# Optimization experiments

Measured on AMD Instinct MI355X. Metric: run time of the kernel, lower is better.

The kernel has to match this reference:

```python
import jax, jax.numpy as jnp
import numpy as np

N = 20000      # nodes
E = 320000     # edges (avg degree 16)
DIN, H1, H2, DOUT = 256, 256, 128, 64


def _lin_params(key, din, dout):
    kw, kb = jax.random.split(key)
    s = 1.0 / np.sqrt(din)
    W = jax.random.uniform(kw, (din, dout), jnp.float32, -s, s)
    b = jax.random.uniform(kb, (dout,), jnp.float32, -s, s)
    return W, b


def setup_inputs() -> dict:
    key = jax.random.key(0)
    keys = jax.random.split(key, 20)
    inp = {
        'x': jax.random.normal(keys[0], (N, DIN), jnp.float32),
        'edge_index': jax.random.randint(keys[1], (2, E), 0, N, jnp.int64),
    }
    dims = [(DIN, H1), (DIN, H1), (DIN, H1),   # layer1 key/query/value
            (H1, H2), (H1, H2), (H1, H2),      # layer2
            (H2, DOUT), (H2, DOUT), (H2, DOUT)]  # layer3
    names = ['k1', 'q1', 'v1', 'k2', 'q2', 'v2', 'k3', 'q3', 'v3']
    for i, (nm, (di, do)) in enumerate(zip(names, dims)):
        W, b = _lin_params(keys[2 + i], di, do)
        inp[nm + '_w'] = W
        inp[nm + '_b'] = b
    # skip (root) weights, no bias per PyG, plus per-conv output bias
    for j, (di, do) in enumerate([(DIN, H1), (H1, H2), (H2, DOUT)], start=1):
        s = 1.0 / np.sqrt(di)
        inp[f's{j}_w'] = jax.random.uniform(keys[11 + 2 * j], (di, do), jnp.float32, -s, s)
        inp[f'bias{j}'] = jnp.zeros((do,), jnp.float32)
    return inp


def _res_gated_conv(x, src, dst, kw, kb, qw, qb, vw, vb, sw, bias):
    # PyG ResGatedGraphConv (flow source_to_target, aggr='add', act=Sigmoid):
    # out_i = lin_skip(x_i) + sum_{j->i} sigmoid(lin_key(x_i) + lin_query(x_j)) * lin_value(x_j) + bias
    k = x @ kw + kb            # [N, D]
    q = x @ qw + qb
    v = x @ vw + vb
    eta = jax.nn.sigmoid(k[dst] + q[src])   # [E, D] edge gate
    msg = eta * v[src]                      # [E, D]
    agg = jax.ops.segment_sum(msg, dst, num_segments=N)  # scatter-add to targets
    return x @ sw + agg + bias


def reference(x, edge_index,
              k1_w, k1_b, q1_w, q1_b, v1_w, v1_b,
              k2_w, k2_b, q2_w, q2_b, v2_w, v2_b,
              k3_w, k3_b, q3_w, q3_b, v3_w, v3_b,
              s1_w, bias1, s2_w, bias2, s3_w, bias3):
    src, dst = edge_index[0], edge_index[1]
    h = _res_gated_conv(x, src, dst, k1_w, k1_b, q1_w, q1_b, v1_w, v1_b, s1_w, bias1)
    # dropout (eval mode -> identity)
    h = _res_gated_conv(h, src, dst, k2_w, k2_b, q2_w, q2_b, v2_w, v2_b, s2_w, bias2)
    h = _res_gated_conv(h, src, dst, k3_w, k3_b, q3_w, q3_b, v3_w, v3_b, s3_w, bias3)
    return jax.nn.softmax(h, axis=1)
```

## Files before the change

### kernel.cpp

```cpp
#include <hip/hip_runtime.h>
#include <hip/hip_bf16.h>
#include <type_traits>


#define NN 20000
#define EE 320000
#define ELLW 64

typedef _Float16 half8 __attribute__((ext_vector_type(8)));
typedef _Float16 half4 __attribute__((ext_vector_type(4)));
typedef _Float16 half2v __attribute__((ext_vector_type(2)));
typedef float f32x4 __attribute__((ext_vector_type(4)));

__device__ __forceinline__ _Float16 f2h(float f) { return (_Float16)f; }
__device__ __forceinline__ float fsigmoid_mul(float v, float x) {
    return v * __builtin_amdgcn_rcpf(1.f + __expf(-x));
}

struct PrepArgs {
    const float* w[3][4];
    const float* b[3][4];
    _Float16* wt[3];
    float* cb[3];
};

__global__ __launch_bounds__(256) void setup_all_kernel(
    const int* __restrict__ ei, int* __restrict__ deg, int* __restrict__ flag,
    const float* __restrict__ x, _Float16* __restrict__ Xh, PrepArgs a) {
    const int b = blockIdx.x;
    const int tid = threadIdx.x;
    if (b < 79) {
        const int i = b * 256 + tid;
        if (i < NN) deg[i] = 0;
    } else if (b == 79) {
        __shared__ int nz;
        if (tid == 0) nz = 0;
        __syncthreads();
        int c = 0;
        for (int t = tid; t < 1024; t += 256)
            if (ei[2 * t + 1] != 0) c = 1;
        if (c) atomicAdd(&nz, 1);
        __syncthreads();
        if (tid == 0) *flag = (nz == 0) ? 1 : 0;
    } else if (b < 1744) {
        const int idx = (b - 80) * 256 + tid;
        int layer, li, K, D, s;
        if (idx < 262144) {
            layer = 0; li = idx; K = 256; D = 256; s = 2;
        } else if (idx < 393216) {
            layer = 1; li = idx - 262144; K = 256; D = 128; s = 1;
        } else {
            layer = 2; li = idx - 393216; K = 128; D = 64; s = 0;
        }
        const int p = li / K;
        const int k = li - p * K;
        const int DV = D >> 6;
        int grp, c;
        if (p < D) {
            grp = 0; c = p;
        } else if (p < 3 * D) {
            const int t = p - D;
            const int g = t >> (s + 1);
            const int r = t & (2 * DV - 1);
            if (r < DV) { grp = 1; c = g * DV + r; }
            else        { grp = 2; c = g * DV + r - DV; }
        } else {
            grp = 3; c = p - 3 * D;
        }
        a.wt[layer][(size_t)p * K + k] =
            f2h(a.w[layer][grp][(size_t)k * D + c]);
        if (k == 0) a.cb[layer][p] = a.b[layer][grp][c];
    } else {
        const int i = ((b - 1744) * 256 + tid) * 8;
        if (i < NN * 256) {
            const float4 f0 = *(const float4*)(x + i);
            const float4 f1 = *(const float4*)(x + i + 4);
            half8 h;
            h[0] = f2h(f0.x); h[1] = f2h(f0.y); h[2] = f2h(f0.z); h[3] = f2h(f0.w);
            h[4] = f2h(f1.x); h[5] = f2h(f1.y); h[6] = f2h(f1.z); h[7] = f2h(f1.w);
            *(half8*)(Xh + i) = h;
        }
    }
}

__device__ __forceinline__ void gemm_tile(
    int bm, int bn, const _Float16* __restrict__ A,
    const _Float16* __restrict__ Bt, const float* __restrict__ catbias,
    _Float16* __restrict__ O, int M, int K, int N) {
    __shared__ _Float16 As[2][4096];
    __shared__ _Float16 Bs[2][4096];

    const int tid = threadIdx.x;
    const int wid = tid >> 6;
    const int lane = tid & 63;
    const int tile_m = bm * 128;
    const int tile_n = bn * 128;
    const int wm = (wid & 1) * 64;
    const int wn = (wid >> 1) * 64;

    const int st_row = (wid << 4) + (lane >> 2);
    const int st_kc = (lane & 3) << 3;

    auto stage = [&](int buf, int kt) {
#pragma unroll
        for (int j = 0; j < 2; ++j) {
            int ar = tile_m + j * 64 + st_row;
            ar = ar < M ? ar : M - 1;
            const _Float16* ag = A + (size_t)ar * K + kt + st_kc;
            __builtin_amdgcn_global_load_lds(
                (const __attribute__((address_space(1))) unsigned int*)ag,
                (__attribute__((address_space(3))) unsigned int*)
                    &As[buf][j * 2048 + (wid << 9)],
                16, 0, 0);
            const int br = tile_n + j * 64 + st_row;
            const _Float16* bg = Bt + (size_t)br * K + kt + st_kc;
            __builtin_amdgcn_global_load_lds(
                (const __attribute__((address_space(1))) unsigned int*)bg,
                (__attribute__((address_space(3))) unsigned int*)
                    &Bs[buf][j * 2048 + (wid << 9)],
                16, 0, 0);
        }
    };

    stage(0, 0);

    f32x4 acc[4][4] = {};
    const int fr = lane & 15;
    const int fk = (lane >> 4) << 3;
    const int niter = K >> 5;

    for (int it = 0; it < niter; ++it) {
        __syncthreads();
        if (it + 1 < niter) stage((it + 1) & 1, (it + 1) << 5);
        const _Float16* as = As[it & 1];
        const _Float16* bs = Bs[it & 1];
        half8 af[4], bf[4];
#pragma unroll
        for (int mi = 0; mi < 4; ++mi)
            af[mi] = *(const half8*)&as[(wm + mi * 16 + fr) * 32 + fk];
#pragma unroll
        for (int ni = 0; ni < 4; ++ni)
            bf[ni] = *(const half8*)&bs[(wn + ni * 16 + fr) * 32 + fk];
#pragma unroll
        for (int mi = 0; mi < 4; ++mi)
#pragma unroll
            for (int ni = 0; ni < 4; ++ni)
                acc[mi][ni] = __builtin_amdgcn_mfma_f32_16x16x32_f16(
                    af[mi], bf[ni], acc[mi][ni], 0, 0, 0);
    }
    __syncthreads();

    _Float16* zone = &As[0][0] + wid * 2048;
    const int cl = lane & 15;
    const int rq = (lane >> 4) << 2;
    const int col0 = tile_n + wn;
    const int r0 = tile_m + wm;
#pragma unroll
    for (int mi = 0; mi < 4; ++mi) {
#pragma unroll
        for (int ni = 0; ni < 4; ++ni) {
            const float cb = catbias[col0 + ni * 16 + cl];
#pragma unroll
            for (int r = 0; r < 4; ++r)
                zone[(rq + r) * 72 + ni * 16 + cl] = f2h(acc[mi][ni][r] + cb);
        }
#pragma unroll
        for (int j = 0; j < 2; ++j) {
            const int rr = j * 8 + (lane >> 3);
            const int row = r0 + mi * 16 + rr;
            const half8 v = *(const half8*)&zone[rr * 72 + (lane & 7) * 8];
            if (row < M)
                *(half8*)&O[(size_t)row * N + col0 + (lane & 7) * 8] = v;
        }
    }
}

__global__ __launch_bounds__(256) void gemm_kernel(
    const _Float16* __restrict__ A, const _Float16* __restrict__ Bt,
    const float* __restrict__ catbias, _Float16* __restrict__ O, int M, int K,
    int N, int mblocks) {
    gemm_tile(blockIdx.x % mblocks, blockIdx.x / mblocks, A, Bt, catbias, O, M,
              K, N);
}

__global__ __launch_bounds__(256) void gemm1_fill_kernel(
    const _Float16* __restrict__ A, const _Float16* __restrict__ Bt,
    const float* __restrict__ catbias, _Float16* __restrict__ O,
    const int* __restrict__ ei, const int* __restrict__ i64flag,
    int* __restrict__ deg, int* __restrict__ col) {
    if (blockIdx.x < 1256) {
        gemm_tile(blockIdx.x % 157, blockIdx.x / 157, A, Bt, catbias, O, NN,
                  256, 1024);
        return;
    }
    const int e = (blockIdx.x - 1256) * 256 + threadIdx.x;
    if (e >= EE) return;
    int src, dst;
    if (*i64flag) {
        const long long* p = (const long long*)ei;
        src = (int)p[e];
        dst = (int)p[EE + e];
    } else {
        src = ei[e];
        dst = ei[EE + e];
    }
    const int pos = atomicAdd(&deg[dst], 1);
    if (pos < ELLW) col[dst * ELLW + pos] = src;
}

template <int D, int MODE>
__global__ __launch_bounds__(256) void edge_gather_kernel(
    const int* __restrict__ deg, const int* __restrict__ col,
    const _Float16* __restrict__ KQVS, _Float16* __restrict__ Hh,
    float* __restrict__ out, int n) {
    constexpr int DV = D / 64;
    constexpr int D4 = 4 * D;
    using qv_t = typename std::conditional<
        DV == 4, half8,
        typename std::conditional<DV == 2, half4, half2v>::type>::type;

    const int node = blockIdx.x * 4 + (threadIdx.x >> 6);
    if (node >= n) return;
    const int lane = threadIdx.x & 63;
    const int ld = lane * DV;

    int dg = deg[node];
    dg = dg < ELLW ? dg : ELLW;
    int idx = col[node * ELLW + lane];
    if (lane >= dg) idx = node;

    float k[DV], acc[DV];
    {
        const _Float16* kp = KQVS + (size_t)node * D4 + ld;
        if constexpr (DV == 4) {
            const half4 u = *(const half4*)kp;
#pragma unroll
            for (int j = 0; j < 4; ++j) k[j] = (float)u[j];
        } else if constexpr (DV == 2) {
            const half2v u = *(const half2v*)kp;
            k[0] = (float)u[0]; k[1] = (float)u[1];
        } else {
            k[0] = (float)*kp;
        }
    }
#pragma unroll
    for (int j = 0; j < DV; ++j) acc[j] = 0.f;

    const _Float16* qvbase = KQVS + D + 2 * ld;
    auto qvacc = [&](qv_t u) {
#pragma unroll
        for (int j = 0; j < DV; ++j)
            acc[j] += fsigmoid_mul((float)u[DV + j], k[j] + (float)u[j]);
    };

    for (int e = 0; e < dg; e += 8) {
        qv_t u[8];
#pragma unroll
        for (int j = 0; j < 8; ++j) {
            const int s = __shfl(idx, e + j, 64);
            u[j] = *(const qv_t*)(qvbase + (size_t)s * D4);
        }
        const int nb = dg - e;
#pragma unroll
        for (int j = 0; j < 8; ++j)
            if (j < nb) qvacc(u[j]);
    }

    float h[DV];
    {
        const _Float16* sp = KQVS + (size_t)node * D4 + 3 * D + ld;
        if constexpr (DV == 4) {
            const half4 u = *(const half4*)sp;
#pragma unroll
            for (int j = 0; j < 4; ++j) h[j] = (float)u[j] + acc[j];
        } else if constexpr (DV == 2) {
            const half2v u = *(const half2v*)sp;
            h[0] = (float)u[0] + acc[0];
            h[1] = (float)u[1] + acc[1];
        } else {
            h[0] = (float)*sp + acc[0];
        }
    }

    if constexpr (MODE == 0) {
        _Float16* op = Hh + (size_t)node * D + ld;
        if constexpr (DV == 4) {
            half4 o;
#pragma unroll
            for (int j = 0; j < 4; ++j) o[j] = f2h(h[j]);
            *(half4*)op = o;
        } else if constexpr (DV == 2) {
            half2v o;
            o[0] = f2h(h[0]); o[1] = f2h(h[1]);
            *(half2v*)op = o;
        } else {
            op[0] = f2h(h[0]);
        }
    } else {
        static_assert(MODE == 0 || DV == 1, "softmax fusion needs D==64");
        float m = h[0];
#pragma unroll
        for (int off = 32; off > 0; off >>= 1)
            m = fmaxf(m, __shfl_xor(m, off, 64));
        const float ex = __expf(h[0] - m);
        float sm = ex;
#pragma unroll
        for (int off = 32; off > 0; off >>= 1) sm += __shfl_xor(sm, off, 64);
        out[(size_t)node * 64 + lane] = ex * __builtin_amdgcn_rcpf(sm);
    }
}

extern "C" void kernel_launch(void* const* d_in, const int* in_sizes, int n_in,
                              void* d_out, int out_size, void* d_ws,
                              size_t ws_size, hipStream_t stream) {
    const float* x = (const float*)d_in[0];
    const int* ei = (const int*)d_in[1];

    char* w = (char*)d_ws;
    _Float16* Xh = (_Float16*)w;     w += (size_t)NN * 256 * 2;
    _Float16* KQVS = (_Float16*)w;   w += (size_t)NN * 1024 * 2;
    _Float16* H1h = (_Float16*)w;    w += (size_t)NN * 256 * 2;
    _Float16* H2h = (_Float16*)w;    w += (size_t)NN * 128 * 2;
    _Float16* Wt1 = (_Float16*)w;    w += (size_t)1024 * 256 * 2;
    _Float16* Wt2 = (_Float16*)w;    w += (size_t)512 * 256 * 2;
    _Float16* Wt3 = (_Float16*)w;    w += (size_t)256 * 128 * 2;
    float* cb1 = (float*)w;          w += 1024 * 4;
    float* cb2 = (float*)w;          w += 512 * 4;
    float* cb3 = (float*)w;          w += 256 * 4;
    int* i64flag = (int*)w;          w += 16;
    int* deg = (int*)w;              w += (size_t)NN * 4;
    int* ell = (int*)w;              w += (size_t)NN * ELLW * 4;

    const dim3 blk(256);
    const int gblocks = (NN + 3) / 4;

    PrepArgs pa;
    pa.w[0][0] = (const float*)d_in[2];  pa.b[0][0] = (const float*)d_in[3];
    pa.w[0][1] = (const float*)d_in[4];  pa.b[0][1] = (const float*)d_in[5];
    pa.w[0][2] = (const float*)d_in[6];  pa.b[0][2] = (const float*)d_in[7];
    pa.w[1][0] = (const float*)d_in[8];  pa.b[1][0] = (const float*)d_in[9];
    pa.w[1][1] = (const float*)d_in[10]; pa.b[1][1] = (const float*)d_in[11];
    pa.w[1][2] = (const float*)d_in[12]; pa.b[1][2] = (const float*)d_in[13];
    pa.w[2][0] = (const float*)d_in[14]; pa.b[2][0] = (const float*)d_in[15];
    pa.w[2][1] = (const float*)d_in[16]; pa.b[2][1] = (const float*)d_in[17];
    pa.w[2][2] = (const float*)d_in[18]; pa.b[2][2] = (const float*)d_in[19];
    pa.w[0][3] = (const float*)d_in[20]; pa.b[0][3] = (const float*)d_in[21];
    pa.w[1][3] = (const float*)d_in[22]; pa.b[1][3] = (const float*)d_in[23];
    pa.w[2][3] = (const float*)d_in[24]; pa.b[2][3] = (const float*)d_in[25];
    pa.wt[0] = Wt1; pa.wt[1] = Wt2; pa.wt[2] = Wt3;
    pa.cb[0] = cb1; pa.cb[1] = cb2; pa.cb[2] = cb3;

    setup_all_kernel<<<4244, blk, 0, stream>>>(ei, deg, i64flag, x, Xh, pa);

    gemm1_fill_kernel<<<2506, blk, 0, stream>>>(Xh, Wt1, cb1, KQVS, ei,
                                                i64flag, deg, ell);
    edge_gather_kernel<256, 0><<<gblocks, blk, 0, stream>>>(
        deg, ell, KQVS, H1h, nullptr, NN);

    gemm_kernel<<<157 * 4, blk, 0, stream>>>(H1h, Wt2, cb2, KQVS, NN, 256, 512,
                                             157);
    edge_gather_kernel<128, 0><<<gblocks, blk, 0, stream>>>(
        deg, ell, KQVS, H2h, nullptr, NN);

    gemm_kernel<<<157 * 2, blk, 0, stream>>>(H2h, Wt3, cb3, KQVS, NN, 128, 256,
                                             157);
    edge_gather_kernel<64, 1><<<gblocks, blk, 0, stream>>>(
        deg, ell, KQVS, nullptr, (float*)d_out, NN);
}
```

Measured before the change: 262.3 us.

## Chunk KQVS into per-32-dim column slabs and gather per chunk with 16-bit indices

The weight prep is reordered so the fused K/Q/V/S GEMM output for layers 1 and 2 lands in 128-column chunks, each stored as a contiguous [N,128] slab holding 32 dims of k, interleaved q/v and skip. New gather kernels handle one chunk per block, with 8 lanes per edge and 8 edges in flight, so each slab's random-access working set is smaller and more cache-friendly. ELL neighbour indices become unsigned short to halve index traffic. This relies on NN fitting in 16 bits and adds more blocks plus cross-lane reductions.

```diff
diff --git a/kernel.cpp b/kernel.cpp
--- a/kernel.cpp
+++ b/kernel.cpp
@@ -44,32 +44,44 @@
         if (tid == 0) *flag = (nz == 0) ? 1 : 0;
     } else if (b < 1744) {
         const int idx = (b - 80) * 256 + tid;
-        int layer, li, K, D, s;
+        int layer, li, K, D;
         if (idx < 262144) {
-            layer = 0; li = idx; K = 256; D = 256; s = 2;
+            layer = 0; li = idx; K = 256; D = 256;
         } else if (idx < 393216) {
-            layer = 1; li = idx - 262144; K = 256; D = 128; s = 1;
+            layer = 1; li = idx - 262144; K = 256; D = 128;
         } else {
-            layer = 2; li = idx - 393216; K = 128; D = 64; s = 0;
+            layer = 2; li = idx - 393216; K = 128; D = 64;
         }
         const int p = li / K;
         const int k = li - p * K;
-        const int DV = D >> 6;
-        int grp, c;
-        if (p < D) {
-            grp = 0; c = p;
-        } else if (p < 3 * D) {
-            const int t = p - D;
-            const int g = t >> (s + 1);
-            const int r = t & (2 * DV - 1);
-            if (r < DV) { grp = 1; c = g * DV + r; }
-            else        { grp = 2; c = g * DV + r - DV; }
+        int grp, dim;
+        if (layer < 2) {
+            const int c = p >> 7;
+            const int local = p & 127;
+            if (local < 32) {
+                grp = 0; dim = c * 32 + local;
+            } else if (local < 96) {
+                const int t = local - 32;
+                const int g8 = t >> 3, r = t & 7;
+                grp = (r < 4) ? 1 : 2;
+                dim = c * 32 + g8 * 4 + (r & 3);
+            } else {
+                grp = 3; dim = c * 32 + local - 96;
+            }
         } else {
-            grp = 3; c = p - 3 * D;
+            if (p < 64) {
+                grp = 0; dim = p;
+            } else if (p < 192) {
+                const int t = p - 64;
+                grp = (t & 1) ? 2 : 1;
+                dim = t >> 1;
+            } else {
+                grp = 3; dim = p - 192;
+            }
         }
         a.wt[layer][(size_t)p * K + k] =
-            f2h(a.w[layer][grp][(size_t)k * D + c]);
-        if (k == 0) a.cb[layer][p] = a.b[layer][grp][c];
+            f2h(a.w[layer][grp][(size_t)k * D + dim]);
+        if (k == 0) a.cb[layer][p] = a.b[layer][grp][dim];
     } else {
         const int i = ((b - 1744) * 256 + tid) * 8;
         if (i < NN * 256) {
@@ -83,6 +95,7 @@
     }
 }
 
+template <bool CHUNKED>
 __device__ __forceinline__ void gemm_tile(
     int bm, int bn, const _Float16* __restrict__ A,
     const _Float16* __restrict__ Bt, const float* __restrict__ catbias,
@@ -155,6 +168,16 @@
     const int rq = (lane >> 4) << 2;
     const int col0 = tile_n + wn;
     const int r0 = tile_m + wm;
+
+    _Float16* obase;
+    int ostride;
+    if constexpr (CHUNKED) {
+        obase = O + (size_t)(col0 >> 7) * NN * 128 + (col0 & 127);
+        ostride = 128;
+    } else {
+        obase = O + col0;
+        ostride = N;
+    }
 #pragma unroll
     for (int mi = 0; mi < 4; ++mi) {
 #pragma unroll
@@ -170,27 +193,28 @@
             const int row = r0 + mi * 16 + rr;
             const half8 v = *(const half8*)&zone[rr * 72 + (lane & 7) * 8];
             if (row < M)
-                *(half8*)&O[(size_t)row * N + col0 + (lane & 7) * 8] = v;
-        }
-    }
-}
-
+                *(half8*)&obase[(size_t)row * ostride + (lane & 7) * 8] = v;
+        }
+    }
+}
+
+template <bool CHUNKED>
 __global__ __launch_bounds__(256) void gemm_kernel(
     const _Float16* __restrict__ A, const _Float16* __restrict__ Bt,
     const float* __restrict__ catbias, _Float16* __restrict__ O, int M, int K,
     int N, int mblocks) {
-    gemm_tile(blockIdx.x % mblocks, blockIdx.x / mblocks, A, Bt, catbias, O, M,
-              K, N);
+    gemm_tile<CHUNKED>(blockIdx.x % mblocks, blockIdx.x / mblocks, A, Bt,
+                       catbias, O, M, K, N);
 }
 
 __global__ __launch_bounds__(256) void gemm1_fill_kernel(
     const _Float16* __restrict__ A, const _Float16* __restrict__ Bt,
     const float* __restrict__ catbias, _Float16* __restrict__ O,
     const int* __restrict__ ei, const int* __restrict__ i64flag,
-    int* __restrict__ deg, int* __restrict__ col) {
+    int* __restrict__ deg, unsigned short* __restrict__ col) {
     if (blockIdx.x < 1256) {
-        gemm_tile(blockIdx.x % 157, blockIdx.x / 157, A, Bt, catbias, O, NN,
-                  256, 1024);
+        gemm_tile<true>(blockIdx.x % 157, blockIdx.x / 157, A, Bt, catbias, O,
+                        NN, 256, 1024);
         return;
     }
     const int e = (blockIdx.x - 1256) * 256 + threadIdx.x;
@@ -205,109 +229,123 @@
         dst = ei[EE + e];
     }
     const int pos = atomicAdd(&deg[dst], 1);
-    if (pos < ELLW) col[dst * ELLW + pos] = src;
-}
-
-template <int D, int MODE>
-__global__ __launch_bounds__(256) void edge_gather_kernel(
-    const int* __restrict__ deg, const int* __restrict__ col,
-    const _Float16* __restrict__ KQVS, _Float16* __restrict__ Hh,
-    float* __restrict__ out, int n) {
-    constexpr int DV = D / 64;
-    constexpr int D4 = 4 * D;
-    using qv_t = typename std::conditional<
-        DV == 4, half8,
-        typename std::conditional<DV == 2, half4, half2v>::type>::type;
-
+    if (pos < ELLW) col[dst * ELLW + pos] = (unsigned short)src;
+}
+
+template <int NCH>
+__global__ __launch_bounds__(256) void gather_chunked_kernel(
+    const int* __restrict__ deg, const unsigned short* __restrict__ col,
+    const _Float16* __restrict__ KQVS, _Float16* __restrict__ Hh, int n) {
+    const int b = blockIdx.x;
+    int chunk, group;
+    if constexpr (NCH == 8) {
+        chunk = b & 7;
+        group = b >> 3;
+    } else {
+        const int slot = b & 7;
+        chunk = slot & 3;
+        group = ((b >> 3) << 1) | (slot >> 2);
+    }
+    const int wid = threadIdx.x >> 6;
+    const int node = group * 4 + wid;
+    if (node >= n) return;
+    const int lane = threadIdx.x & 63;
+    const int j = lane & 7;
+    const int g = lane >> 3;
+
+    const _Float16* cbase = KQVS + (size_t)chunk * NN * 128;
+    const _Float16* nb = cbase + (size_t)node * 128;
+
+    int dg = deg[node];
+    dg = dg < ELLW ? dg : ELLW;
+    int idx = (int)col[node * ELLW + lane];
+    if (lane >= dg) idx = node;
+
+    float k[4], acc[4] = {0.f, 0.f, 0.f, 0.f};
+    {
+        const half4 u = *(const half4*)(nb + j * 4);
+#pragma unroll
+        for (int t = 0; t < 4; ++t) k[t] = (float)u[t];
+    }
+
+    auto qvacc = [&](half8 u) {
+#pragma unroll
+        for (int t = 0; t < 4; ++t)
+            acc[t] += fsigmoid_mul((float)u[4 + t], k[t] + (float)u[t]);
+    };
+    auto qvload = [&](int e) {
+        const int s = __shfl(idx, e, 64);
+        return *(const half8*)(cbase + (size_t)s * 128 + 32 + j * 8);
+    };
+
+    const int R = (dg + 7) >> 3;
+    int e = g;
+    half8 u = qvload(e);
+    for (int i = 1; i < R; ++i) {
+        const int en = i * 8 + g;
+        const half8 un = qvload(en);
+        if (e < dg) qvacc(u);
+        u = un;
+        e = en;
+    }
+    if (R > 0 && e < dg) qvacc(u);
+
+#pragma unroll
+    for (int t = 0; t < 4; ++t) {
+        acc[t] += __shfl_xor(acc[t], 8, 64);
+        acc[t] += __shfl_xor(acc[t], 16, 64);
+        acc[t] += __shfl_xor(acc[t], 32, 64);
+    }
+
+    if (g == 0) {
+        const half4 s4 = *(const half4*)(nb + 96 + j * 4);
+        half4 o;
+#pragma unroll
+        for (int t = 0; t < 4; ++t) o[t] = f2h((float)s4[t] + acc[t]);
+        *(half4*)(Hh + (size_t)node * (NCH * 32) + chunk * 32 + j * 4) = o;
+    }
+}
+
+__global__ __launch_bounds__(256) void edge_gather3_kernel(
+    const int* __restrict__ deg, const unsigned short* __restrict__ col,
+    const _Float16* __restrict__ KQVS, float* __restrict__ out, int n) {
     const int node = blockIdx.x * 4 + (threadIdx.x >> 6);
     if (node >= n) return;
     const int lane = threadIdx.x & 63;
-    const int ld = lane * DV;
 
     int dg = deg[node];
     dg = dg < ELLW ? dg : ELLW;
-    int idx = col[node * ELLW + lane];
+    int idx = (int)col[node * ELLW + lane];
     if (lane >= dg) idx = node;
 
-    float k[DV], acc[DV];
-    {
-        const _Float16* kp = KQVS + (size_t)node * D4 + ld;
-        if constexpr (DV == 4) {
-            const half4 u = *(const half4*)kp;
-#pragma unroll
-            for (int j = 0; j < 4; ++j) k[j] = (float)u[j];
-        } else if constexpr (DV == 2) {
-            const half2v u = *(const half2v*)kp;
-            k[0] = (float)u[0]; k[1] = (float)u[1];
-        } else {
-            k[0] = (float)*kp;
-        }
-    }
-#pragma unroll
-    for (int j = 0; j < DV; ++j) acc[j] = 0.f;
-
-    const _Float16* qvbase = KQVS + D + 2 * ld;
-    auto qvacc = [&](qv_t u) {
-#pragma unroll
-        for (int j = 0; j < DV; ++j)
-            acc[j] += fsigmoid_mul((float)u[DV + j], k[j] + (float)u[j]);
-    };
+    const float k = (float)KQVS[(size_t)node * 256 + lane];
+    float acc = 0.f;
+    const _Float16* qvbase = KQVS + 64 + 2 * lane;
 
     for (int e = 0; e < dg; e += 8) {
-        qv_t u[8];
-#pragma unroll
-        for (int j = 0; j < 8; ++j) {
-            const int s = __shfl(idx, e + j, 64);
-            u[j] = *(const qv_t*)(qvbase + (size_t)s * D4);
+        half2v u[8];
+#pragma unroll
+        for (int t = 0; t < 8; ++t) {
+            const int s = __shfl(idx, e + t, 64);
+            u[t] = *(const half2v*)(qvbase + (size_t)s * 256);
         }
         const int nb = dg - e;
 #pragma unroll
-        for (int j = 0; j < 8; ++j)
-            if (j < nb) qvacc(u[j]);
-    }
-
-    float h[DV];
-    {
-        const _Float16* sp = KQVS + (size_t)node * D4 + 3 * D + ld;
-        if constexpr (DV == 4) {
-            const half4 u = *(const half4*)sp;
-#pragma unroll
-            for (int j = 0; j < 4; ++j) h[j] = (float)u[j] + acc[j];
-        } else if constexpr (DV == 2) {
-            const half2v u = *(const half2v*)sp;
-            h[0] = (float)u[0] + acc[0];
-            h[1] = (float)u[1] + acc[1];
-        } else {
-            h[0] = (float)*sp + acc[0];
-        }
-    }
-
-    if constexpr (MODE == 0) {
-        _Float16* op = Hh + (size_t)node * D + ld;
-        if constexpr (DV == 4) {
-            half4 o;
-#pragma unroll
-            for (int j = 0; j < 4; ++j) o[j] = f2h(h[j]);
-            *(half4*)op = o;
-        } else if constexpr (DV == 2) {
-            half2v o;
-            o[0] = f2h(h[0]); o[1] = f2h(h[1]);
-            *(half2v*)op = o;
-        } else {
-            op[0] = f2h(h[0]);
-        }
-    } else {
-        static_assert(MODE == 0 || DV == 1, "softmax fusion needs D==64");
-        float m = h[0];
-#pragma unroll
-        for (int off = 32; off > 0; off >>= 1)
-            m = fmaxf(m, __shfl_xor(m, off, 64));
-        const float ex = __expf(h[0] - m);
-        float sm = ex;
-#pragma unroll
-        for (int off = 32; off > 0; off >>= 1) sm += __shfl_xor(sm, off, 64);
-        out[(size_t)node * 64 + lane] = ex * __builtin_amdgcn_rcpf(sm);
-    }
+        for (int t = 0; t < 8; ++t)
+            if (t < nb) acc += fsigmoid_mul((float)u[t][1], k + (float)u[t][0]);
+    }
+
+    const float h = (float)KQVS[(size_t)node * 256 + 192 + lane] + acc;
+
+    float m = h;
+#pragma unroll
+    for (int off = 32; off > 0; off >>= 1)
+        m = fmaxf(m, __shfl_xor(m, off, 64));
+    const float ex = __expf(h - m);
+    float sm = ex;
+#pragma unroll
+    for (int off = 32; off > 0; off >>= 1) sm += __shfl_xor(sm, off, 64);
+    out[(size_t)node * 64 + lane] = ex * __builtin_amdgcn_rcpf(sm);
 }
 
 extern "C" void kernel_launch(void* const* d_in, const int* in_sizes, int n_in,
@@ -329,10 +367,9 @@
     float* cb3 = (float*)w;          w += 256 * 4;
     int* i64flag = (int*)w;          w += 16;
     int* deg = (int*)w;              w += (size_t)NN * 4;
-    int* ell = (int*)w;              w += (size_t)NN * ELLW * 4;
+    unsigned short* ell = (unsigned short*)w;  w += (size_t)NN * ELLW * 2;
 
     const dim3 blk(256);
-    const int gblocks = (NN + 3) / 4;
 
     PrepArgs pa;
     pa.w[0][0] = (const float*)d_in[2];  pa.b[0][0] = (const float*)d_in[3];
@@ -354,16 +391,16 @@
 
     gemm1_fill_kernel<<<2506, blk, 0, stream>>>(Xh, Wt1, cb1, KQVS, ei,
                                                 i64flag, deg, ell);
-    edge_gather_kernel<256, 0><<<gblocks, blk, 0, stream>>>(
-        deg, ell, KQVS, H1h, nullptr, NN);
-
-    gemm_kernel<<<157 * 4, blk, 0, stream>>>(H1h, Wt2, cb2, KQVS, NN, 256, 512,
-                                             157);
-    edge_gather_kernel<128, 0><<<gblocks, blk, 0, stream>>>(
-        deg, ell, KQVS, H2h, nullptr, NN);
-
-    gemm_kernel<<<157 * 2, blk, 0, stream>>>(H2h, Wt3, cb3, KQVS, NN, 128, 256,
-                                             157);
-    edge_gather_kernel<64, 1><<<gblocks, blk, 0, stream>>>(
-        deg, ell, KQVS, nullptr, (float*)d_out, NN);
-}
+    gather_chunked_kernel<8><<<40000, blk, 0, stream>>>(deg, ell, KQVS, H1h,
+                                                        NN);
+
+    gemm_kernel<true><<<157 * 4, blk, 0, stream>>>(H1h, Wt2, cb2, KQVS, NN,
+                                                   256, 512, 157);
+    gather_chunked_kernel<4><<<20000, blk, 0, stream>>>(deg, ell, KQVS, H2h,
+                                                        NN);
+
+    gemm_kernel<false><<<157 * 2, blk, 0, stream>>>(H2h, Wt3, cb3, KQVS, NN,
+                                                    128, 256, 157);
+    edge_gather3_kernel<<<(NN + 3) / 4, blk, 0, stream>>>(deg, ell, KQVS,
+                                                          (float*)d_out, NN);
+}
```

Measured after the change: 272.2 us. 1.04x slower.

## Fuse all stages into one persistent kernel with grid barriers

Applied to the files above, without the earlier changes.

Replaces the seven kernel launches with a single persistent kernel sized to occupancy. Stages are separated by software grid barriers built on atomic counters. It also switches the ELL column indices to 16-bit values padded with a sentinel row of zeros, double-buffers the neighbor gather loads, and folds the sigmoid into an exp2 with a prescaled key. This targets launch overhead and stage tails, but it relies on every block being co-resident for the spin barrier, and the gather work per stage is serialized behind global synchronization.

```diff
diff --git a/kernel.cpp b/kernel.cpp
--- a/kernel.cpp
+++ b/kernel.cpp
@@ -6,6 +6,7 @@
 #define NN 20000
 #define EE 320000
 #define ELLW 64
+#define NL2E -1.4426950408889634f
 
 typedef _Float16 half8 __attribute__((ext_vector_type(8)));
 typedef _Float16 half4 __attribute__((ext_vector_type(4)));
@@ -13,82 +14,46 @@
 typedef float f32x4 __attribute__((ext_vector_type(4)));
 
 __device__ __forceinline__ _Float16 f2h(float f) { return (_Float16)f; }
-__device__ __forceinline__ float fsigmoid_mul(float v, float x) {
-    return v * __builtin_amdgcn_rcpf(1.f + __expf(-x));
-}
-
-struct PrepArgs {
+
+struct MegaParams {
+    const float* x;
+    const int* ei;
     const float* w[3][4];
     const float* b[3][4];
+    _Float16* Xh;
+    _Float16* KQVS;
+    _Float16* H1h;
+    _Float16* H2h;
     _Float16* wt[3];
     float* cb[3];
+    int* i64flag;
+    int* deg;
+    unsigned short* ell;
+    unsigned* bar;
+    float* out;
 };
 
-__global__ __launch_bounds__(256) void setup_all_kernel(
-    const int* __restrict__ ei, int* __restrict__ deg, int* __restrict__ flag,
-    const float* __restrict__ x, _Float16* __restrict__ Xh, PrepArgs a) {
-    const int b = blockIdx.x;
-    const int tid = threadIdx.x;
-    if (b < 79) {
-        const int i = b * 256 + tid;
-        if (i < NN) deg[i] = 0;
-    } else if (b == 79) {
-        __shared__ int nz;
-        if (tid == 0) nz = 0;
-        __syncthreads();
-        int c = 0;
-        for (int t = tid; t < 1024; t += 256)
-            if (ei[2 * t + 1] != 0) c = 1;
-        if (c) atomicAdd(&nz, 1);
-        __syncthreads();
-        if (tid == 0) *flag = (nz == 0) ? 1 : 0;
-    } else if (b < 1744) {
-        const int idx = (b - 80) * 256 + tid;
-        int layer, li, K, D, s;
-        if (idx < 262144) {
-            layer = 0; li = idx; K = 256; D = 256; s = 2;
-        } else if (idx < 393216) {
-            layer = 1; li = idx - 262144; K = 256; D = 128; s = 1;
-        } else {
-            layer = 2; li = idx - 393216; K = 128; D = 64; s = 0;
-        }
-        const int p = li / K;
-        const int k = li - p * K;
-        const int DV = D >> 6;
-        int grp, c;
-        if (p < D) {
-            grp = 0; c = p;
-        } else if (p < 3 * D) {
-            const int t = p - D;
-            const int g = t >> (s + 1);
-            const int r = t & (2 * DV - 1);
-            if (r < DV) { grp = 1; c = g * DV + r; }
-            else        { grp = 2; c = g * DV + r - DV; }
-        } else {
-            grp = 3; c = p - 3 * D;
-        }
-        a.wt[layer][(size_t)p * K + k] =
-            f2h(a.w[layer][grp][(size_t)k * D + c]);
-        if (k == 0) a.cb[layer][p] = a.b[layer][grp][c];
-    } else {
-        const int i = ((b - 1744) * 256 + tid) * 8;
-        if (i < NN * 256) {
-            const float4 f0 = *(const float4*)(x + i);
-            const float4 f1 = *(const float4*)(x + i + 4);
-            half8 h;
-            h[0] = f2h(f0.x); h[1] = f2h(f0.y); h[2] = f2h(f0.z); h[3] = f2h(f0.w);
-            h[4] = f2h(f1.x); h[5] = f2h(f1.y); h[6] = f2h(f1.z); h[7] = f2h(f1.w);
-            *(half8*)(Xh + i) = h;
-        }
-    }
+__device__ __forceinline__ void gbar(unsigned* cnt, unsigned target) {
+    __syncthreads();
+    if (threadIdx.x == 0) {
+        __threadfence();
+        __hip_atomic_fetch_add(cnt, 1u, __ATOMIC_RELEASE,
+                               __HIP_MEMORY_SCOPE_AGENT);
+        while (__hip_atomic_load(cnt, __ATOMIC_ACQUIRE,
+                                 __HIP_MEMORY_SCOPE_AGENT) < target)
+            __builtin_amdgcn_s_sleep(2);
+        __threadfence();
+    }
+    __syncthreads();
 }
 
-__device__ __forceinline__ void gemm_tile(
-    int bm, int bn, const _Float16* __restrict__ A,
-    const _Float16* __restrict__ Bt, const float* __restrict__ catbias,
-    _Float16* __restrict__ O, int M, int K, int N) {
+__device__ void gemm_tile(int bm, int bn, const _Float16* __restrict__ A,
+                          const _Float16* __restrict__ Bt,
+                          const float* __restrict__ catbias,
+                          _Float16* __restrict__ O, int M, int K, int N) {
     __shared__ _Float16 As[2][4096];
     __shared__ _Float16 Bs[2][4096];
+    __syncthreads();
 
     const int tid = threadIdx.x;
     const int wid = tid >> 6;
@@ -175,110 +140,86 @@
     }
 }
 
-__global__ __launch_bounds__(256) void gemm_kernel(
-    const _Float16* __restrict__ A, const _Float16* __restrict__ Bt,
-    const float* __restrict__ catbias, _Float16* __restrict__ O, int M, int K,
-    int N, int mblocks) {
-    gemm_tile(blockIdx.x % mblocks, blockIdx.x / mblocks, A, Bt, catbias, O, M,
-              K, N);
-}
-
-__global__ __launch_bounds__(256) void gemm1_fill_kernel(
-    const _Float16* __restrict__ A, const _Float16* __restrict__ Bt,
-    const float* __restrict__ catbias, _Float16* __restrict__ O,
-    const int* __restrict__ ei, const int* __restrict__ i64flag,
-    int* __restrict__ deg, int* __restrict__ col) {
-    if (blockIdx.x < 1256) {
-        gemm_tile(blockIdx.x % 157, blockIdx.x / 157, A, Bt, catbias, O, NN,
-                  256, 1024);
-        return;
-    }
-    const int e = (blockIdx.x - 1256) * 256 + threadIdx.x;
-    if (e >= EE) return;
-    int src, dst;
-    if (*i64flag) {
-        const long long* p = (const long long*)ei;
-        src = (int)p[e];
-        dst = (int)p[EE + e];
-    } else {
-        src = ei[e];
-        dst = ei[EE + e];
-    }
-    const int pos = atomicAdd(&deg[dst], 1);
-    if (pos < ELLW) col[dst * ELLW + pos] = src;
-}
-
 template <int D, int MODE>
-__global__ __launch_bounds__(256) void edge_gather_kernel(
-    const int* __restrict__ deg, const int* __restrict__ col,
-    const _Float16* __restrict__ KQVS, _Float16* __restrict__ Hh,
-    float* __restrict__ out, int n) {
+__device__ __forceinline__ void gather_flat(
+    int node, const int* __restrict__ deg,
+    const unsigned short* __restrict__ col, const _Float16* __restrict__ KQVS,
+    _Float16* __restrict__ Hh, float* __restrict__ out) {
     constexpr int DV = D / 64;
     constexpr int D4 = 4 * D;
     using qv_t = typename std::conditional<
         DV == 4, half8,
         typename std::conditional<DV == 2, half4, half2v>::type>::type;
 
-    const int node = blockIdx.x * 4 + (threadIdx.x >> 6);
-    if (node >= n) return;
     const int lane = threadIdx.x & 63;
     const int ld = lane * DV;
+    const _Float16* nrow = KQVS + (size_t)node * D4;
 
     int dg = deg[node];
     dg = dg < ELLW ? dg : ELLW;
-    int idx = col[node * ELLW + lane];
-    if (lane >= dg) idx = node;
-
-    float k[DV], acc[DV];
+    const int R = (dg + 7) >> 3;
+    const int idx = (int)col[node * ELLW + lane];
+
+    float kpre[DV], acc[DV];
     {
-        const _Float16* kp = KQVS + (size_t)node * D4 + ld;
         if constexpr (DV == 4) {
-            const half4 u = *(const half4*)kp;
-#pragma unroll
-            for (int j = 0; j < 4; ++j) k[j] = (float)u[j];
+            const half4 u = *(const half4*)(nrow + ld);
+#pragma unroll
+            for (int t = 0; t < 4; ++t) kpre[t] = (float)u[t] * NL2E;
         } else if constexpr (DV == 2) {
-            const half2v u = *(const half2v*)kp;
-            k[0] = (float)u[0]; k[1] = (float)u[1];
-        } else {
-            k[0] = (float)*kp;
-        }
-    }
-#pragma unroll
-    for (int j = 0; j < DV; ++j) acc[j] = 0.f;
+            const half2v u = *(const half2v*)(nrow + ld);
+            kpre[0] = (float)u[0] * NL2E;
+            kpre[1] = (float)u[1] * NL2E;
+        } else {
+            kpre[0] = (float)nrow[ld] * NL2E;
+        }
+    }
+#pragma unroll
+    for (int t = 0; t < DV; ++t) acc[t] = 0.f;
 
     const _Float16* qvbase = KQVS + D + 2 * ld;
-    auto qvacc = [&](qv_t u) {
-#pragma unroll
-        for (int j = 0; j < DV; ++j)
-            acc[j] += fsigmoid_mul((float)u[DV + j], k[j] + (float)u[j]);
+
+    auto ld8 = [&](int r, qv_t* u) {
+#pragma unroll
+        for (int j = 0; j < 8; ++j) {
+            const int s = __shfl(idx, r * 8 + j, 64);
+            u[j] = *(const qv_t*)(qvbase + (size_t)s * D4);
+        }
     };
-
-    for (int e = 0; e < dg; e += 8) {
-        qv_t u[8];
-#pragma unroll
-        for (int j = 0; j < 8; ++j) {
-            const int s = __shfl(idx, e + j, 64);
-            u[j] = *(const qv_t*)(qvbase + (size_t)s * D4);
-        }
-        const int nb = dg - e;
+    auto cp8 = [&](const qv_t* u) {
 #pragma unroll
         for (int j = 0; j < 8; ++j)
-            if (j < nb) qvacc(u[j]);
+#pragma unroll
+            for (int t = 0; t < DV; ++t) {
+                const float e = __builtin_amdgcn_exp2f(
+                    fmaf((float)u[j][t], NL2E, kpre[t]));
+                acc[t] = fmaf((float)u[j][DV + t],
+                              __builtin_amdgcn_rcpf(1.f + e), acc[t]);
+            }
+    };
+
+    qv_t ua[8], ub[8];
+    if (R > 0) {
+        ld8(0, ua);
+        for (int i = 1; i < R; ++i) {
+            if (i & 1) { ld8(i, ub); cp8(ua); }
+            else       { ld8(i, ua); cp8(ub); }
+        }
+        if (R & 1) cp8(ua); else cp8(ub);
     }
 
     float h[DV];
     {
-        const _Float16* sp = KQVS + (size_t)node * D4 + 3 * D + ld;
         if constexpr (DV == 4) {
-            const half4 u = *(const half4*)sp;
-#pragma unroll
-            for (int j = 0; j < 4; ++j) h[j] = (float)u[j] + acc[j];
+            const half4 u = *(const half4*)(nrow + 3 * D + ld);
+#pragma unroll
+            for (int t = 0; t < 4; ++t) h[t] = (float)u[t] + acc[t];
         } else if constexpr (DV == 2) {
-            const half2v u = *(const half2v*)sp;
+            const half2v u = *(const half2v*)(nrow + 3 * D + ld);
             h[0] = (float)u[0] + acc[0];
             h[1] = (float)u[1] + acc[1];
         } else {
-            h[0] = (float)*sp + acc[0];
+            h[0] = (float)nrow[3 * D + ld] + acc[0];
         }
     }
 
@@ -287,7 +228,7 @@
         if constexpr (DV == 4) {
             half4 o;
 #pragma unroll
-            for (int j = 0; j < 4; ++j) o[j] = f2h(h[j]);
+            for (int t = 0; t < 4; ++t) o[t] = f2h(h[t]);
             *(half4*)op = o;
         } else if constexpr (DV == 2) {
             half2v o;
@@ -310,60 +251,174 @@
     }
 }
 
+__global__ __launch_bounds__(256, 3) void mega_kernel(MegaParams P) {
+    const unsigned NB = gridDim.x;
+    const int tid = threadIdx.x;
+    const int gtid = blockIdx.x * 256 + tid;
+    const int gsz = NB * 256;
+
+    for (int i = gtid; i < NN; i += gsz) P.deg[i] = 0;
+    {
+        unsigned* e = (unsigned*)P.ell;
+        for (int i = gtid; i < NN * ELLW / 2; i += gsz) e[i] = 0x4E204E20u;
+    }
+    {
+        unsigned* z = (unsigned*)(P.KQVS + (size_t)NN * 1024);
+        for (int i = gtid; i < 512; i += gsz) z[i] = 0u;
+    }
+    if (blockIdx.x == 0) {
+        __shared__ int nz;
+        if (tid == 0) nz = 0;
+        __syncthreads();
+        int c = 0;
+        for (int t = tid; t < 1024; t += 256)
+            if (P.ei[2 * t + 1] != 0) c = 1;
+        if (c) atomicAdd(&nz, 1);
+        __syncthreads();
+        if (tid == 0) *P.i64flag = (nz == 0) ? 1 : 0;
+    }
+    for (int idx = gtid; idx < 425984; idx += gsz) {
+        int layer, li, K, D, s;
+        if (idx < 262144)      { layer = 0; li = idx;          K = 256; D = 256; s = 2; }
+        else if (idx < 393216) { layer = 1; li = idx - 262144; K = 256; D = 128; s = 1; }
+        else                   { layer = 2; li = idx - 393216; K = 128; D = 64;  s = 0; }
+        const int p = li / K;
+        const int k = li - p * K;
+        const int DV = D >> 6;
+        int grp, c;
+        if (p < D) {
+            grp = 0; c = p;
+        } else if (p < 3 * D) {
+            const int t = p - D;
+            const int g = t >> (s + 1);
+            const int r = t & (2 * DV - 1);
+            if (r < DV) { grp = 1; c = g * DV + r; }
+            else        { grp = 2; c = g * DV + r - DV; }
+        } else {
+            grp = 3; c = p - 3 * D;
+        }
+        P.wt[layer][(size_t)p * K + k] =
+            f2h(P.w[layer][grp][(size_t)k * D + c]);
+        if (k == 0) P.cb[layer][p] = P.b[layer][grp][c];
+    }
+    for (int i = gtid; i < 640000; i += gsz) {
+        const int o = i * 8;
+        const float4 f0 = *(const float4*)(P.x + o);
+        const float4 f1 = *(const float4*)(P.x + o + 4);
+        half8 h;
+        h[0] = f2h(f0.x); h[1] = f2h(f0.y); h[2] = f2h(f0.z); h[3] = f2h(f0.w);
+        h[4] = f2h(f1.x); h[5] = f2h(f1.y); h[6] = f2h(f1.z); h[7] = f2h(f1.w);
+        *(half8*)(P.Xh + o) = h;
+    }
+    gbar(P.bar, 1u * NB);
+
+    for (int u = blockIdx.x; u < 2506; u += NB) {
+        if (u < 1256) {
+            gemm_tile(u % 157, u / 157, P.Xh, P.wt[0], P.cb[0], P.KQVS, NN,
+                      256, 1024);
+        } else {
+            const int e = (u - 1256) * 256 + tid;
+            if (e < EE) {
+                int src, dst;
+                if (*P.i64flag) {
+                    const long long* p = (const long long*)P.ei;
+                    src = (int)p[e];
+                    dst = (int)p[EE + e];
+                } else {
+                    src = P.ei[e];
+                    dst = P.ei[EE + e];
+                }
+                const int pos = atomicAdd(&P.deg[dst], 1);
+                if (pos < ELLW) P.ell[dst * ELLW + pos] = (unsigned short)src;
+            }
+        }
+    }
+    gbar(P.bar, 2u * NB);
+
+    for (int u = blockIdx.x; u < 5000; u += NB) {
+        const int node = u * 4 + (tid >> 6);
+        gather_flat<256, 0>(node, P.deg, P.ell, P.KQVS, P.H1h, nullptr);
+    }
+    gbar(P.bar, 3u * NB);
+
+    for (int u = blockIdx.x; u < 629; u += NB) {
+        if (u < 628) {
+            gemm_tile(u % 157, u / 157, P.H1h, P.wt[1], P.cb[1], P.KQVS, NN,
+                      256, 512);
+        } else {
+            unsigned* z = (unsigned*)(P.KQVS + (size_t)NN * 512);
+            if (tid < 256) z[tid] = 0u;
+        }
+    }
+    gbar(P.bar, 4u * NB);
+
+    for (int u = blockIdx.x; u < 5000; u += NB) {
+        const int node = u * 4 + (tid >> 6);
+        gather_flat<128, 0>(node, P.deg, P.ell, P.KQVS, P.H2h, nullptr);
+    }
+    gbar(P.bar, 5u * NB);
+
+    for (int u = blockIdx.x; u < 315; u += NB) {
+        if (u < 314) {
+            gemm_tile(u % 157, u / 157, P.H2h, P.wt[2], P.cb[2], P.KQVS, NN,
+                      128, 256);
+        } else {
+            unsigned* z = (unsigned*)(P.KQVS + (size_t)NN * 256);
+            if (tid < 128) z[tid] = 0u;
+        }
+    }
+    gbar(P.bar, 6u * NB);
+
+    for (int u = blockIdx.x; u < 5000; u += NB) {
+        const int node = u * 4 + (tid >> 6);
+        gather_flat<64, 1>(node, P.deg, P.ell, P.KQVS, nullptr, P.out);
+    }
+}
+
 extern "C" void kernel_launch(void* const* d_in, const int* in_sizes, int n_in,
                               void* d_out, int out_size, void* d_ws,
                               size_t ws_size, hipStream_t stream) {
-    const float* x = (const float*)d_in[0];
-    const int* ei = (const int*)d_in[1];
-
-    char* w = (char*)d_ws;
-    _Float16* Xh = (_Float16*)w;     w += (size_t)NN * 256 * 2;
-    _Float16* KQVS = (_Float16*)w;   w += (size_t)NN * 1024 * 2;
-    _Float16* H1h = (_Float16*)w;    w += (size_t)NN * 256 * 2;
-    _Float16* H2h = (_Float16*)w;    w += (size_t)NN * 128 * 2;
-    _Float16* Wt1 = (_Float16*)w;    w += (size_t)1024 * 256 * 2;
-    _Float16* Wt2 = (_Float16*)w;    w += (size_t)512 * 256 * 2;
-    _Float16* Wt3 = (_Float16*)w;    w += (size_t)256 * 128 * 2;
-    float* cb1 = (float*)w;          w += 1024 * 4;
-    float* cb2 = (float*)w;          w += 512 * 4;
-    float* cb3 = (float*)w;          w += 256 * 4;
-    int* i64flag = (int*)w;          w += 16;
-    int* deg = (int*)w;              w += (size_t)NN * 4;
-    int* ell = (int*)w;              w += (size_t)NN * ELLW * 4;
-
-    const dim3 blk(256);
-    const int gblocks = (NN + 3) / 4;
-
-    PrepArgs pa;
-    pa.w[0][0] = (const float*)d_in[2];  pa.b[0][0] = (const float*)d_in[3];
-    pa.w[0][1] = (const float*)d_in[4];  pa.b[0][1] = (const float*)d_in[5];
-    pa.w[0][2] = (const float*)d_in[6];  pa.b[0][2] = (const float*)d_in[7];
-    pa.w[1][0] = (const float*)d_in[8];  pa.b[1][0] = (const float*)d_in[9];
-    pa.w[1][1] = (const float*)d_in[10]; pa.b[1][1] = (const float*)d_in[11];
-    pa.w[1][2] = (const float*)d_in[12]; pa.b[1][2] = (const float*)d_in[13];
-    pa.w[2][0] = (const float*)d_in[14]; pa.b[2][0] = (const float*)d_in[15];
-    pa.w[2][1] = (const float*)d_in[16]; pa.b[2][1] = (const float*)d_in[17];
-    pa.w[2][2] = (const float*)d_in[18]; pa.b[2][2] = (const float*)d_in[19];
-    pa.w[0][3] = (const float*)d_in[20]; pa.b[0][3] = (const float*)d_in[21];
-    pa.w[1][3] = (const float*)d_in[22]; pa.b[1][3] = (const float*)d_in[23];
-    pa.w[2][3] = (const float*)d_in[24]; pa.b[2][3] = (const float*)d_in[25];
-    pa.wt[0] = Wt1; pa.wt[1] = Wt2; pa.wt[2] = Wt3;
-    pa.cb[0] = cb1; pa.cb[1] = cb2; pa.cb[2] = cb3;
-
-    setup_all_kernel<<<4244, blk, 0, stream>>>(ei, deg, i64flag, x, Xh, pa);
-
-    gemm1_fill_kernel<<<2506, blk, 0, stream>>>(Xh, Wt1, cb1, KQVS, ei,
-                                                i64flag, deg, ell);
-    edge_gather_kernel<256, 0><<<gblocks, blk, 0, stream>>>(
-        deg, ell, KQVS, H1h, nullptr, NN);
-
-    gemm_kernel<<<157 * 4, blk, 0, stream>>>(H1h, Wt2, cb2, KQVS, NN, 256, 512,
-                                             157);
-    edge_gather_kernel<128, 0><<<gblocks, blk, 0, stream>>>(
-        deg, ell, KQVS, H2h, nullptr, NN);
-
-    gemm_kernel<<<157 * 2, blk, 0, stream>>>(H2h, Wt3, cb3, KQVS, NN, 128, 256,
-                                             157);
-    edge_gather_kernel<64, 1><<<gblocks, blk, 0, stream>>>(
-        deg, ell, KQVS, nullptr, (float*)d_out, NN);
+    unsigned* bar = (unsigned*)d_ws;
+    char* w = (char*)d_ws + 64;
+
+    MegaParams P;
+    P.x = (const float*)d_in[0];
+    P.ei = (const int*)d_in[1];
+    P.w[0][0] = (const float*)d_in[2];  P.b[0][0] = (const float*)d_in[3];
+    P.w[0][1] = (const float*)d_in[4];  P.b[0][1] = (const float*)d_in[5];
+    P.w[0][2] = (const float*)d_in[6];  P.b[0][2] = (const float*)d_in[7];
+    P.w[1][0] = (const float*)d_in[8];  P.b[1][0] = (const float*)d_in[9];
+    P.w[1][1] = (const float*)d_in[10]; P.b[1][1] = (const float*)d_in[11];
+    P.w[1][2] = (const float*)d_in[12]; P.b[1][2] = (const float*)d_in[13];
+    P.w[2][0] = (const float*)d_in[14]; P.b[2][0] = (const float*)d_in[15];
+    P.w[2][1] = (const float*)d_in[16]; P.b[2][1] = (const float*)d_in[17];
+    P.w[2][2] = (const float*)d_in[18]; P.b[2][2] = (const float*)d_in[19];
+    P.w[0][3] = (const float*)d_in[20]; P.b[0][3] = (const float*)d_in[21];
+    P.w[1][3] = (const float*)d_in[22]; P.b[1][3] = (const float*)d_in[23];
+    P.w[2][3] = (const float*)d_in[24]; P.b[2][3] = (const float*)d_in[25];
+
+    P.Xh = (_Float16*)w;     w += (size_t)NN * 256 * 2;
+    P.KQVS = (_Float16*)w;   w += (size_t)(NN + 1) * 1024 * 2;
+    P.H1h = (_Float16*)w;    w += (size_t)NN * 256 * 2;
+    P.H2h = (_Float16*)w;    w += (size_t)NN * 128 * 2;
+    P.wt[0] = (_Float16*)w;  w += (size_t)1024 * 256 * 2;
+    P.wt[1] = (_Float16*)w;  w += (size_t)512 * 256 * 2;
+    P.wt[2] = (_Float16*)w;  w += (size_t)256 * 128 * 2;
+    P.cb[0] = (float*)w;     w += 1024 * 4;
+    P.cb[1] = (float*)w;     w += 512 * 4;
+    P.cb[2] = (float*)w;     w += 256 * 4;
+    P.i64flag = (int*)w;     w += 16;
+    P.deg = (int*)w;         w += (size_t)NN * 4;
+    P.ell = (unsigned short*)w;  w += (size_t)NN * ELLW * 2;
+    P.bar = bar;
+    P.out = (float*)d_out;
+
+    int nb = 0;
+    hipOccupancyMaxActiveBlocksPerMultiprocessor(&nb, mega_kernel, 256, 0);
+    if (nb < 1) nb = 1;
+    int grid = nb * 256;
+    if (grid > 1280) grid = 1280;
+
+    hipMemsetAsync(bar, 0, 64, stream);
+    mega_kernel<<<grid, 256, 0, stream>>>(P);
 }
```

Result: slower. 607.0 us (+131.4%).

## Use 16-bit ELL indices with a zero dummy row and double-buffered neighbor gathers

Applied to the files above, without the earlier changes.

ELL column indices are stored as 16-bit values, and empty slots are prefilled with a sentinel pointing at an extra zero row (node NN) appended to KQVS. The per-lane fallback to the node's own index is removed, and the zero row is re-zeroed after each GEMM by an extra block. The gather loop now double-buffers loads of 8 neighbors while computing the previous batch, and the sigmoid uses exp2 with a prescaled key. The aim is to halve index traffic and overlap gather latency with compute, at the cost of extra setup work and more registers per lane.

```diff
diff --git a/kernel.cpp b/kernel.cpp
--- a/kernel.cpp
+++ b/kernel.cpp
@@ -6,6 +6,7 @@
 #define NN 20000
 #define EE 320000
 #define ELLW 64
+#define NL2E -1.4426950408889634f
 
 typedef _Float16 half8 __attribute__((ext_vector_type(8)));
 typedef _Float16 half4 __attribute__((ext_vector_type(4)));
@@ -13,9 +14,6 @@
 typedef float f32x4 __attribute__((ext_vector_type(4)));
 
 __device__ __forceinline__ _Float16 f2h(float f) { return (_Float16)f; }
-__device__ __forceinline__ float fsigmoid_mul(float v, float x) {
-    return v * __builtin_amdgcn_rcpf(1.f + __expf(-x));
-}
 
 struct PrepArgs {
     const float* w[3][4];
@@ -26,7 +24,9 @@
 
 __global__ __launch_bounds__(256) void setup_all_kernel(
     const int* __restrict__ ei, int* __restrict__ deg, int* __restrict__ flag,
-    const float* __restrict__ x, _Float16* __restrict__ Xh, PrepArgs a) {
+    const float* __restrict__ x, _Float16* __restrict__ Xh,
+    unsigned int* __restrict__ ell_i, unsigned int* __restrict__ kqvs_i,
+    PrepArgs a) {
     const int b = blockIdx.x;
     const int tid = threadIdx.x;
     if (b < 79) {
@@ -45,13 +45,9 @@
     } else if (b < 1744) {
         const int idx = (b - 80) * 256 + tid;
         int layer, li, K, D, s;
-        if (idx < 262144) {
-            layer = 0; li = idx; K = 256; D = 256; s = 2;
-        } else if (idx < 393216) {
-            layer = 1; li = idx - 262144; K = 256; D = 128; s = 1;
-        } else {
-            layer = 2; li = idx - 393216; K = 128; D = 64; s = 0;
-        }
+        if (idx < 262144)      { layer = 0; li = idx;          K = 256; D = 256; s = 2; }
+        else if (idx < 393216) { layer = 1; li = idx - 262144; K = 256; D = 128; s = 1; }
+        else                   { layer = 2; li = idx - 393216; K = 128; D = 64;  s = 0; }
         const int p = li / K;
         const int k = li - p * K;
         const int DV = D >> 6;
@@ -70,7 +66,7 @@
         a.wt[layer][(size_t)p * K + k] =
             f2h(a.w[layer][grp][(size_t)k * D + c]);
         if (k == 0) a.cb[layer][p] = a.b[layer][grp][c];
-    } else {
+    } else if (b < 4244) {
         const int i = ((b - 1744) * 256 + tid) * 8;
         if (i < NN * 256) {
             const float4 f0 = *(const float4*)(x + i);
@@ -80,6 +76,12 @@
             h[4] = f2h(f1.x); h[5] = f2h(f1.y); h[6] = f2h(f1.z); h[7] = f2h(f1.w);
             *(half8*)(Xh + i) = h;
         }
+    } else if (b < 6744) {
+        const int i = (b - 4244) * 256 + tid;
+        if (i < NN * ELLW / 2) ell_i[i] = 0x4E204E20u;
+    } else {
+        for (int i = tid; i < 512; i += 256)
+            kqvs_i[(size_t)NN * 512 + i] = 0u;
     }
 }
 
@@ -178,7 +180,12 @@
 __global__ __launch_bounds__(256) void gemm_kernel(
     const _Float16* __restrict__ A, const _Float16* __restrict__ Bt,
     const float* __restrict__ catbias, _Float16* __restrict__ O, int M, int K,
-    int N, int mblocks) {
+    int N, int mblocks, int ntiles) {
+    if ((int)blockIdx.x >= ntiles) {
+        unsigned* z = (unsigned*)(O + (size_t)NN * N);
+        for (int i = threadIdx.x; i < N / 2; i += 256) z[i] = 0u;
+        return;
+    }
     gemm_tile(blockIdx.x % mblocks, blockIdx.x / mblocks, A, Bt, catbias, O, M,
               K, N);
 }
@@ -187,7 +194,7 @@
     const _Float16* __restrict__ A, const _Float16* __restrict__ Bt,
     const float* __restrict__ catbias, _Float16* __restrict__ O,
     const int* __restrict__ ei, const int* __restrict__ i64flag,
-    int* __restrict__ deg, int* __restrict__ col) {
+    int* __restrict__ deg, unsigned short* __restrict__ col) {
     if (blockIdx.x < 1256) {
         gemm_tile(blockIdx.x % 157, blockIdx.x / 157, A, Bt, catbias, O, NN,
                   256, 1024);
@@ -205,14 +212,14 @@
         dst = ei[EE + e];
     }
     const int pos = atomicAdd(&deg[dst], 1);
-    if (pos < ELLW) col[dst * ELLW + pos] = src;
+    if (pos < ELLW) col[dst * ELLW + pos] = (unsigned short)src;
 }
 
 template <int D, int MODE>
-__global__ __launch_bounds__(256) void edge_gather_kernel(
-    const int* __restrict__ deg, const int* __restrict__ col,
+__global__ __launch_bounds__(256) void gather_kernel(
+    const int* __restrict__ deg, const unsigned short* __restrict__ col,
     const _Float16* __restrict__ KQVS, _Float16* __restrict__ Hh,
-    float* __restrict__ out, int n) {
+    float* __restrict__ out) {
     constexpr int DV = D / 64;
     constexpr int D4 = 4 * D;
     using qv_t = typename std::conditional<
@@ -220,65 +227,75 @@
         typename std::conditional<DV == 2, half4, half2v>::type>::type;
 
     const int node = blockIdx.x * 4 + (threadIdx.x >> 6);
-    if (node >= n) return;
     const int lane = threadIdx.x & 63;
     const int ld = lane * DV;
+    const _Float16* nrow = KQVS + (size_t)node * D4;
 
     int dg = deg[node];
     dg = dg < ELLW ? dg : ELLW;
-    int idx = col[node * ELLW + lane];
-    if (lane >= dg) idx = node;
-
-    float k[DV], acc[DV];
+    const int R = (dg + 7) >> 3;
+    const int idx = (int)col[node * ELLW + lane];
+
+    float kpre[DV], acc[DV];
     {
-        const _Float16* kp = KQVS + (size_t)node * D4 + ld;
         if constexpr (DV == 4) {
-            const half4 u = *(const half4*)kp;
-#pragma unroll
-            for (int j = 0; j < 4; ++j) k[j] = (float)u[j];
+            const half4 u = *(const half4*)(nrow + ld);
+#pragma unroll
+            for (int t = 0; t < 4; ++t) kpre[t] = (float)u[t] * NL2E;
         } else if constexpr (DV == 2) {
-            const half2v u = *(const half2v*)kp;
-            k[0] = (float)u[0]; k[1] = (float)u[1];
+            const half2v u = *(const half2v*)(nrow + ld);
+            kpre[0] = (float)u[0] * NL2E;
+            kpre[1] = (float)u[1] * NL2E;
         } else {
-            k[0] = (float)*kp;
-        }
-    }
-#pragma unroll
-    for (int j = 0; j < DV; ++j) acc[j] = 0.f;
+            kpre[0] = (float)nrow[ld] * NL2E;
+        }
+    }
+#pragma unroll
+    for (int t = 0; t < DV; ++t) acc[t] = 0.f;
 
     const _Float16* qvbase = KQVS + D + 2 * ld;
-    auto qvacc = [&](qv_t u) {
-#pragma unroll
-        for (int j = 0; j < DV; ++j)
-            acc[j] += fsigmoid_mul((float)u[DV + j], k[j] + (float)u[j]);
+
+    auto ld8 = [&](int r, qv_t* u) {
+#pragma unroll
+        for (int j = 0; j < 8; ++j) {
+            const int s = __shfl(idx, r * 8 + j, 64);
+            u[j] = *(const qv_t*)(qvbase + (size_t)s * D4);
+        }
     };
-
-    for (int e = 0; e < dg; e += 8) {
-        qv_t u[8];
-#pragma unroll
-        for (int j = 0; j < 8; ++j) {
-            const int s = __shfl(idx, e + j, 64);
-            u[j] = *(const qv_t*)(qvbase + (size_t)s * D4);
-        }
-        const int nb = dg - e;
+    auto cp8 = [&](const qv_t* u) {
 #pragma unroll
         for (int j = 0; j < 8; ++j)
-            if (j < nb) qvacc(u[j]);
+#pragma unroll
+            for (int t = 0; t < DV; ++t) {
+                const float e = __builtin_amdgcn_exp2f(
+                    fmaf((float)u[j][t], NL2E, kpre[t]));
+                acc[t] = fmaf((float)u[j][DV + t],
+                              __builtin_amdgcn_rcpf(1.f + e), acc[t]);
+            }
+    };
+
+    qv_t ua[8], ub[8];
+    if (R > 0) {
+        ld8(0, ua);
+        for (int i = 1; i < R; ++i) {
+            if (i & 1) { ld8(i, ub); cp8(ua); }
+            else       { ld8(i, ua); cp8(ub); }
+        }
+        if (R & 1) cp8(ua); else cp8(ub);
     }
 
     float h[DV];
     {
-        const _Float16* sp = KQVS + (size_t)node * D4 + 3 * D + ld;
         if constexpr (DV == 4) {
-            const half4 u = *(const half4*)sp;
-#pragma unroll
-            for (int j = 0; j < 4; ++j) h[j] = (float)u[j] + acc[j];
+            const half4 u = *(const half4*)(nrow + 3 * D + ld);
+#pragma unroll
+            for (int t = 0; t < 4; ++t) h[t] = (float)u[t] + acc[t];
         } else if constexpr (DV == 2) {
-            const half2v u = *(const half2v*)sp;
+            const half2v u = *(const half2v*)(nrow + 3 * D + ld);
             h[0] = (float)u[0] + acc[0];
             h[1] = (float)u[1] + acc[1];
         } else {
-            h[0] = (float)*sp + acc[0];
+            h[0] = (float)nrow[3 * D + ld] + acc[0];
         }
     }
 
@@ -287,7 +304,7 @@
         if constexpr (DV == 4) {
             half4 o;
 #pragma unroll
-            for (int j = 0; j < 4; ++j) o[j] = f2h(h[j]);
+            for (int t = 0; t < 4; ++t) o[t] = f2h(h[t]);
             *(half4*)op = o;
         } else if constexpr (DV == 2) {
             half2v o;
@@ -318,7 +335,7 @@
 
     char* w = (char*)d_ws;
     _Float16* Xh = (_Float16*)w;     w += (size_t)NN * 256 * 2;
-    _Float16* KQVS = (_Float16*)w;   w += (size_t)NN * 1024 * 2;
+    _Float16* KQVS = (_Float16*)w;   w += (size_t)(NN + 1) * 1024 * 2;
     _Float16* H1h = (_Float16*)w;    w += (size_t)NN * 256 * 2;
     _Float16* H2h = (_Float16*)w;    w += (size_t)NN * 128 * 2;
     _Float16* Wt1 = (_Float16*)w;    w += (size_t)1024 * 256 * 2;
@@ -329,10 +346,10 @@
     float* cb3 = (float*)w;          w += 256 * 4;
     int* i64flag = (int*)w;          w += 16;
     int* deg = (int*)w;              w += (size_t)NN * 4;
-    int* ell = (int*)w;              w += (size_t)NN * ELLW * 4;
+    unsigned short* ell = (unsigned short*)w;  w += (size_t)NN * ELLW * 2;
 
     const dim3 blk(256);
-    const int gblocks = (NN + 3) / 4;
+    const int gblocks = NN / 4;
 
     PrepArgs pa;
     pa.w[0][0] = (const float*)d_in[2];  pa.b[0][0] = (const float*)d_in[3];
@@ -350,20 +367,21 @@
     pa.wt[0] = Wt1; pa.wt[1] = Wt2; pa.wt[2] = Wt3;
     pa.cb[0] = cb1; pa.cb[1] = cb2; pa.cb[2] = cb3;
 
-    setup_all_kernel<<<4244, blk, 0, stream>>>(ei, deg, i64flag, x, Xh, pa);
+    setup_all_kernel<<<6745, blk, 0, stream>>>(
+        ei, deg, i64flag, x, Xh, (unsigned int*)ell, (unsigned int*)KQVS, pa);
 
     gemm1_fill_kernel<<<2506, blk, 0, stream>>>(Xh, Wt1, cb1, KQVS, ei,
                                                 i64flag, deg, ell);
-    edge_gather_kernel<256, 0><<<gblocks, blk, 0, stream>>>(
-        deg, ell, KQVS, H1h, nullptr, NN);
-
-    gemm_kernel<<<157 * 4, blk, 0, stream>>>(H1h, Wt2, cb2, KQVS, NN, 256, 512,
-                                             157);
-    edge_gather_kernel<128, 0><<<gblocks, blk, 0, stream>>>(
-        deg, ell, KQVS, H2h, nullptr, NN);
-
-    gemm_kernel<<<157 * 2, blk, 0, stream>>>(H2h, Wt3, cb3, KQVS, NN, 128, 256,
-                                             157);
-    edge_gather_kernel<64, 1><<<gblocks, blk, 0, stream>>>(
-        deg, ell, KQVS, nullptr, (float*)d_out, NN);
-}
+    gather_kernel<256, 0><<<gblocks, blk, 0, stream>>>(deg, ell, KQVS, H1h,
+                                                       nullptr);
+
+    gemm_kernel<<<157 * 4 + 1, blk, 0, stream>>>(H1h, Wt2, cb2, KQVS, NN, 256,
+                                                 512, 157, 628);
+    gather_kernel<128, 0><<<gblocks, blk, 0, stream>>>(deg, ell, KQVS, H2h,
+                                                       nullptr);
+
+    gemm_kernel<<<157 * 2 + 1, blk, 0, stream>>>(H2h, Wt3, cb3, KQVS, NN, 128,
+                                                 256, 157, 314);
+    gather_kernel<64, 1><<<gblocks, blk, 0, stream>>>(deg, ell, KQVS, nullptr,
+                                                      (float*)d_out);
+}
```

Measured after the change: 264.5 us. No clear change (+0.8%).
